# Kernel optimization log

Measured on AMD Instinct MI355X. Metric: run time of the kernel, lower is better.

Reference implementation:

```python
import jax, jax.numpy as jnp
import numpy as np
from jax import lax

B, HI, WI, D = 8, 64, 64, 128
HO, WO = HI // 2, WI // 2
N_IN, N_OUT = HI * WI, HO * WO
NUM_ITERS = 3
EPS = 1e-6


def _build_indices(Ho, Wo):
    # replicates _build_q_and_in_idx: per coarse position, 9 relative offsets
    dys = np.repeat(np.arange(-1, 2), 3)
    dxs = np.tile(np.arange(-1, 2), 3)
    oy = np.arange(Ho)[:, None, None]
    ox = np.arange(Wo)[None, :, None]
    ny = oy + dys
    nx = ox + dxs
    valid = (ny >= 0) & (ny < Ho) & (nx >= 0) & (nx < Wo)  # (Ho,Wo,9)
    coarse = np.where(valid, ny * Wo + nx, 0)
    base = (oy * Wo + ox) * 9
    g9 = np.where(valid, base + np.arange(9), 0).reshape(-1, 9)
    c9 = coarse.reshape(-1, 9)
    q_idx = np.stack([np.tile(g9, (1, 4))] * 4)
    col_idx = np.stack([np.tile(c9, (1, 4))] * 4)
    in_idx = np.stack([np.tile(np.where(valid, coarse * 4 + h, 0).reshape(-1, 9), (1, 4)) for h in range(4)])
    return q_idx.astype(np.int32), in_idx.astype(np.int32), col_idx.astype(np.int32)


Q_IDX, IN_IDX, COL_IDX = _build_indices(HO, WO)
# NATTEN kernel-3 neighborhoods: window center clamped to stay in-bounds.
NY = np.clip(np.arange(HO) - 1, 0, HO - 3)[:, None] + np.arange(3)  # (HO,3)
NX = np.clip(np.arange(WO) - 1, 0, WO - 3)[:, None] + np.arange(3)  # (WO,3)


def _ln(x, g, b, eps=1e-5):
    mu = x.mean(-1, keepdims=True)
    var = ((x - mu) ** 2).mean(-1, keepdims=True)
    return (x - mu) * lax.rsqrt(var + eps) * g + b


def _forward(x, seed_w, wq, wk, wv, w1, b1, w2, b2, ln_in_g, ln_in_b, ln_out_g, ln_out_b, rpb, tau):
    ny, nx = jnp.asarray(NY), jnp.asarray(NX)
    q_idx = jnp.asarray(Q_IDX)

    def unfold(t):  # (B,HI,WI,D) -> (B,4,HO,WO,D); head = ky*2+kx (F.unfold order)
        return t.reshape(B, HO, 2, WO, 2, D).transpose(0, 2, 4, 1, 3, 5).reshape(B, 4, HO, WO, D)

    k = unfold((_ln(x, ln_in_g, ln_in_b) @ wk.T).reshape(B, HI, WI, D))
    v = unfold((x @ wv.T).reshape(B, HI, WI, D))
    k_n = k[:, :, ny][:, :, :, :, nx]  # (B,4,HO,3,WO,3,D)
    v_n = v[:, :, ny][:, :, :, :, nx]

    x_map = x.reshape(B, HI, WI, D).transpose(0, 3, 1, 2)
    seed = lax.conv_general_dilated(x_map, seed_w, (2, 2), ((1, 1), (1, 1)),
                                    dimension_numbers=('NCHW', 'OIHW', 'NCHW'))
    x_out = _ln(seed.reshape(B, D, N_OUT).transpose(0, 2, 1), ln_out_g, ln_out_b)

    scale = jnp.exp(tau)
    attn36 = a_col_h = None
    for _ in range(NUM_ITERS):
        q = (_ln(x_out, ln_out_g, ln_out_b) @ wq.T).reshape(B, HO, WO, D)
        # na2d_qk (q broadcast over the 4 heads) + relative position bias
        logits = jnp.einsum('byxd,bhykxld->bhyxkl', q, k_n).reshape(B, 4, HO, WO, 9) + rpb.reshape(1, 4, 1, 1, 9)
        attn = jax.nn.softmax(logits * scale, axis=-1) + EPS
        flat = attn.reshape(B, 4, N_OUT * 9)
        attn36 = jnp.take_along_axis(
            flat, jnp.broadcast_to(q_idx.reshape(1, 4, -1), (B, 4, N_OUT * 36)), axis=-1
        ).reshape(B, 4, N_OUT, 36)
        a_col_h = attn36 / (attn36.sum(axis=(1, 3), keepdims=True) + EPS)
        attn9 = a_col_h[..., :9].reshape(B, 4, HO, WO, 3, 3)
        # na2d_av then sum over heads
        updates = jnp.einsum('bhyxkl,bhykxld->byxd', attn9, v_n).reshape(B, N_OUT, D)
        x_out = x_out + updates
        h1 = jax.nn.gelu(x_out @ w1.T + b1, approximate=False)
        x_out = x_out + _ln(h1 @ w2.T + b2, ln_out_g, ln_out_b)
    return x_out, attn36, a_col_h


def setup_inputs() -> dict:
    key = jax.random.key(0)
    ks = jax.random.split(key, 8)
    n = lambda k, shape, s: jax.random.normal(k, shape, jnp.float32) * s
    D2 = 2 * D
    return {
        'x': jax.random.normal(ks[0], (B, N_IN, D), jnp.float32),
        'seed_w': n(ks[1], (D, D, 3, 3), (2.0 / (9 * D)) ** 0.5),
        'wq': n(ks[2], (D, D), D ** -0.5),
        'wk': n(ks[3], (D, D), D ** -0.5),
        'wv': n(ks[4], (D, D), D ** -0.5),
        'w1': n(ks[5], (D2, D), D ** -0.5),
        'b1': jnp.zeros((D2,), jnp.float32),
        'w2': n(ks[6], (D, D2), D2 ** -0.5),
        'b2': jnp.zeros((D,), jnp.float32),
        'ln_in_g': jnp.ones((D,), jnp.float32),
        'ln_in_b': jnp.zeros((D,), jnp.float32),
        'ln_out_g': jnp.ones((D,), jnp.float32),
        'ln_out_b': jnp.zeros((D,), jnp.float32),
        'rpb': n(ks[7], (4, 9), 0.02),
        'tau': jnp.float32(np.log(D ** -0.5)),
    }


def reference(x, seed_w, wq, wk, wv, w1, b1, w2, b2, ln_in_g, ln_in_b, ln_out_g, ln_out_b, rpb, tau):
    x_out, attn36, a_col_h = _forward(x, seed_w, wq, wk, wv, w1, b1, w2, b2,
                                      ln_in_g, ln_in_b, ln_out_g, ln_out_b, rpb, tau)
    # A_col: scatter_add over dim 1 -> A_col[b, in_idx[i,j], j] += a_col_h[b,i,j]
    rows = jnp.asarray(IN_IDX).reshape(4 * N_OUT, 36)
    cols = jnp.broadcast_to(jnp.arange(36), rows.shape)
    A_col = jnp.zeros((B, N_IN, N_OUT), x.dtype).at[:, rows, cols].add(a_col_h.reshape(B, 4 * N_OUT, 36))
    # A_row: scatter_add over dim 2 -> A_row[b, i, col_idx[i,j]] += attn36[b,i,j]
    ri = jnp.broadcast_to(jnp.arange(4 * N_OUT)[:, None], (4 * N_OUT, 36))
    A_row = jnp.zeros((B, N_IN, N_OUT), x.dtype).at[:, ri, jnp.asarray(COL_IDX).reshape(4 * N_OUT, 36)].add(
        attn36.reshape(B, 4 * N_OUT, 36))
    return x_out, A_row, A_col
```

## Files before the change

kernel.cpp:

```cpp
#include <hip/hip_runtime.h>
#include <hip/hip_bf16.h>
#include <math.h>

#define BB   8
#define HI_  64
#define WI_  64
#define DD   128
#define HO_  32
#define WO_  32
#define NIN  4096
#define NOUT 1024
#define LN_EPS 1e-5f
#define ATT_EPS 1e-6f

#define ZSHARE 3932160

typedef short bf16x8 __attribute__((ext_vector_type(8)));
typedef float f32x4  __attribute__((ext_vector_type(4)));

__device__ __forceinline__ ushort f2bf(float f) {
    union { float f; unsigned u; } a; a.f = f;
    unsigned u = a.u;
    return (ushort)((u + 0x7FFFu + ((u >> 16) & 1u)) >> 16);
}
__device__ __forceinline__ float bf2f(ushort u) {
    union { unsigned u; float f; } a; a.u = ((unsigned)u) << 16;
    return a.f;
}

__global__ __launch_bounds__(256)
void wconvert_kernel(const float* __restrict__ wq, const float* __restrict__ wk,
                     const float* __restrict__ wv, const float* __restrict__ w1,
                     const float* __restrict__ w2, const float* __restrict__ sw,
                     ushort* __restrict__ dst)
{
    int i = blockIdx.x * 256 + threadIdx.x;
    float v;
    if (i < 16384)        v = wk[i];
    else if (i < 32768)   v = wv[i - 16384];
    else if (i < 49152) { int j = i - 32768; int d = j >> 7, n = j & 127;
                          v = wq[n * DD + d]; }
    else if (i < 81920)   v = w1[i - 49152];
    else if (i < 114688)  v = w2[i - 81920];
    else {
        int j = i - 114688;
        int n = j / 1152;
        int rem = j - n * 1152;
        int tap = rem >> 7, di = rem & 127;
        v = sw[((size_t)(n * DD + di)) * 9 + tap];
    }
    dst[i] = f2bf(v);
}

__global__ __launch_bounds__(256)
void prep_kernel(const float* __restrict__ x, const ushort* __restrict__ wkb,
                 const ushort* __restrict__ wvb, const ushort* __restrict__ wqTb,
                 const ushort* __restrict__ wcb,
                 const float* __restrict__ ligg, const float* __restrict__ libb,
                 const float* __restrict__ logg, const float* __restrict__ lobb,
                 ushort* __restrict__ k2buf, ushort* __restrict__ vbuf,
                 float* __restrict__ xout, float4* __restrict__ zb)
{
    __shared__ __align__(16) char arena[35328];
    const int tid = threadIdx.x;
    const int wid = tid >> 6, lane = tid & 63;
    const int lr = lane & 15, lk = (lane >> 4) << 3;

    {
        float4* zp = zb + (size_t)blockIdx.x * 3840;
        float4 zz = make_float4(0.f, 0.f, 0.f, 0.f);
        #pragma unroll
        for (int i = 0; i < 15; ++i) zp[i * 256 + tid] = zz;
    }

    if (blockIdx.x < 512) {
        ushort (*Araw)[136] = (ushort (*)[136])(arena);
        ushort (*Aln)[136]  = (ushort (*)[136])(arena + 17408);
        const int row0 = blockIdx.x * 64;

        #pragma unroll
        for (int i = 0; i < 8; ++i) {
            int l = tid + i * 256;
            int r = l >> 5, c4 = (l & 31) << 2;
            float4 v = *(const float4*)(x + (size_t)(row0 + r) * DD + c4);
            ushort4 o; o.x = f2bf(v.x); o.y = f2bf(v.y); o.z = f2bf(v.z); o.w = f2bf(v.w);
            *(ushort4*)&Araw[r][c4] = o;
            float s  = v.x + v.y + v.z + v.w;
            float s2 = v.x * v.x + v.y * v.y + v.z * v.z + v.w * v.w;
            #pragma unroll
            for (int o2 = 16; o2 > 0; o2 >>= 1) {
                s  += __shfl_down(s,  o2, 32);
                s2 += __shfl_down(s2, o2, 32);
            }
            s  = __shfl(s,  0, 32);
            s2 = __shfl(s2, 0, 32);
            float mu = s * (1.f / DD);
            float rs = rsqrtf(s2 * (1.f / DD) - mu * mu + LN_EPS);
            ushort4 o2v;
            o2v.x = f2bf((v.x - mu) * rs * ligg[c4 + 0] + libb[c4 + 0]);
            o2v.y = f2bf((v.y - mu) * rs * ligg[c4 + 1] + libb[c4 + 1]);
            o2v.z = f2bf((v.z - mu) * rs * ligg[c4 + 2] + libb[c4 + 2]);
            o2v.w = f2bf((v.w - mu) * rs * ligg[c4 + 3] + libb[c4 + 3]);
            *(ushort4*)&Aln[r][c4] = o2v;
        }
        __syncthreads();

        const int wm = (wid & 1) * 32, wn = (wid >> 1) * 64;
        {
            f32x4 ak[2][4] = {}, av[2][4] = {};
            #pragma unroll
            for (int ks = 0; ks < 4; ++ks) {
                int kk = ks * 32 + lk;
                bf16x8 aL[2], aR[2];
                #pragma unroll
                for (int mi = 0; mi < 2; ++mi) {
                    aL[mi] = *(const bf16x8*)&Aln[wm + mi * 16 + lr][kk];
                    aR[mi] = *(const bf16x8*)&Araw[wm + mi * 16 + lr][kk];
                }
                #pragma unroll
                for (int ni = 0; ni < 4; ++ni) {
                    bf16x8 bK = *(const bf16x8*)(wkb + (size_t)(wn + ni * 16 + lr) * DD + kk);
                    bf16x8 bV = *(const bf16x8*)(wvb + (size_t)(wn + ni * 16 + lr) * DD + kk);
                    #pragma unroll
                    for (int mi = 0; mi < 2; ++mi) {
                        ak[mi][ni] = __builtin_amdgcn_mfma_f32_16x16x32_bf16(aL[mi], bK, ak[mi][ni], 0, 0, 0);
                        av[mi][ni] = __builtin_amdgcn_mfma_f32_16x16x32_bf16(aR[mi], bV, av[mi][ni], 0, 0, 0);
                    }
                }
            }
            #pragma unroll
            for (int mi = 0; mi < 2; ++mi)
                #pragma unroll
                for (int ni = 0; ni < 4; ++ni) {
                    int n = wn + ni * 16 + (lane & 15);
                    #pragma unroll
                    for (int r = 0; r < 4; ++r) {
                        int m = row0 + wm + mi * 16 + ((lane >> 4) << 2) + r;
                        int b = m >> 12, pix = m & 4095;
                        int iy = pix >> 6, ix = pix & 63;
                        int h = ((iy & 1) << 1) | (ix & 1);
                        int cp = ((iy >> 1) << 5) | (ix >> 1);
                        size_t orow = ((size_t)(b * 4 + h) << 10) + cp;
                        vbuf[orow * DD + n] = f2bf(av[mi][ni][r]);
                    }
                }
            __syncthreads();
            #pragma unroll
            for (int mi = 0; mi < 2; ++mi)
                #pragma unroll
                for (int ni = 0; ni < 4; ++ni) {
                    int n = wn + ni * 16 + (lane & 15);
                    #pragma unroll
                    for (int r = 0; r < 4; ++r) {
                        int lm = wm + mi * 16 + ((lane >> 4) << 2) + r;
                        Aln[lm][n] = f2bf(ak[mi][ni][r]);
                    }
                }
        }
        __syncthreads();

        {
            f32x4 a2[2][4] = {};
            #pragma unroll
            for (int ks = 0; ks < 4; ++ks) {
                int kk = ks * 32 + lk;
                bf16x8 aF[2];
                aF[0] = *(const bf16x8*)&Aln[wm + lr][kk];
                aF[1] = *(const bf16x8*)&Aln[wm + 16 + lr][kk];
                #pragma unroll
                for (int ni = 0; ni < 4; ++ni) {
                    bf16x8 bF = *(const bf16x8*)(wqTb + (size_t)(wn + ni * 16 + lr) * DD + kk);
                    a2[0][ni] = __builtin_amdgcn_mfma_f32_16x16x32_bf16(aF[0], bF, a2[0][ni], 0, 0, 0);
                    a2[1][ni] = __builtin_amdgcn_mfma_f32_16x16x32_bf16(aF[1], bF, a2[1][ni], 0, 0, 0);
                }
            }
            #pragma unroll
            for (int mi = 0; mi < 2; ++mi)
                #pragma unroll
                for (int ni = 0; ni < 4; ++ni) {
                    int n = wn + ni * 16 + (lane & 15);
                    #pragma unroll
                    for (int r = 0; r < 4; ++r) {
                        int m = row0 + wm + mi * 16 + ((lane >> 4) << 2) + r;
                        int b = m >> 12, pix = m & 4095;
                        int iy = pix >> 6, ix = pix & 63;
                        int h = ((iy & 1) << 1) | (ix & 1);
                        int cp = ((iy >> 1) << 5) | (ix >> 1);
                        size_t orow = ((size_t)(b * 4 + h) << 10) + cp;
                        k2buf[orow * DD + n] = f2bf(a2[mi][ni][r]);
                    }
                }
        }
    } else {
        ushort (*As)[72]   = (ushort (*)[72])(arena);
        ushort (*Bs)[72]   = (ushort (*)[72])(arena + 2304);
        float  (*es)[132]  = (float  (*)[132])(arena + 20736);
        float  (*rstat)[2] = (float  (*)[2])(arena + 29184);
        const int row0 = (blockIdx.x - 512) * 16;
        const int wn = wid * 32;
        f32x4 acc[2] = {};

        for (int k0 = 0; k0 < 1152; k0 += 64) {
            {
                int r = tid >> 4, c4 = (tid & 15) << 2;
                int m = row0 + r;
                int b = m >> 10, p = m & 1023;
                int y = p >> 5, xx = p & 31;
                int kg = k0 + c4;
                int tap = kg >> 7, di = kg & 127;
                int ky = tap / 3, kx = tap - ky * 3;
                int iy = 2 * y + ky - 1, ix = 2 * xx + kx - 1;
                float4 v;
                if ((unsigned)iy < (unsigned)HI_ && (unsigned)ix < (unsigned)WI_)
                    v = *(const float4*)(x + ((size_t)b * NIN + iy * WI_ + ix) * DD + di);
                else v = make_float4(0.f, 0.f, 0.f, 0.f);
                ushort4 o; o.x = f2bf(v.x); o.y = f2bf(v.y); o.z = f2bf(v.z); o.w = f2bf(v.w);
                *(ushort4*)&As[r][c4] = o;
            }
            #pragma unroll
            for (int i = 0; i < 4; ++i) {
                int l = tid + i * 256;
                int r = l >> 3, c8 = (l & 7) << 3;
                *(uint4*)&Bs[r][c8] = *(const uint4*)(wcb + (size_t)r * 1152 + k0 + c8);
            }
            __syncthreads();
            #pragma unroll
            for (int ks = 0; ks < 2; ++ks) {
                int kk = ks * 32 + lk;
                bf16x8 a0 = *(const bf16x8*)&As[lr][kk];
                #pragma unroll
                for (int ni = 0; ni < 2; ++ni) {
                    bf16x8 bF = *(const bf16x8*)&Bs[wn + ni * 16 + lr][kk];
                    acc[ni] = __builtin_amdgcn_mfma_f32_16x16x32_bf16(a0, bF, acc[ni], 0, 0, 0);
                }
            }
            __syncthreads();
        }
        #pragma unroll
        for (int ni = 0; ni < 2; ++ni) {
            int n = wn + ni * 16 + (lane & 15);
            #pragma unroll
            for (int r = 0; r < 4; ++r)
                es[((lane >> 4) << 2) + r][n] = acc[ni][r];
        }
        __syncthreads();
        if (tid < 64) {
            int r = tid >> 2, q = tid & 3;
            float s = 0.f, s2 = 0.f;
            #pragma unroll
            for (int c = 0; c < 32; ++c) { float v = es[r][q * 32 + c]; s += v; s2 += v * v; }
            s += __shfl_down(s, 1, 64); s2 += __shfl_down(s2, 1, 64);
            s += __shfl_down(s, 2, 64); s2 += __shfl_down(s2, 2, 64);
            if (q == 0) {
                float mu = s * (1.f / DD);
                float var = s2 * (1.f / DD) - mu * mu;
                rstat[r][0] = mu; rstat[r][1] = rsqrtf(var + LN_EPS);
            }
        }
        __syncthreads();
        #pragma unroll
        for (int i = 0; i < 2; ++i) {
            int l = tid + i * 256;
            int r = l >> 5, c4 = (l & 31) << 2;
            float mu = rstat[r][0], rs = rstat[r][1];
            float4 o;
            o.x = (es[r][c4 + 0] - mu) * rs * logg[c4 + 0] + lobb[c4 + 0];
            o.y = (es[r][c4 + 1] - mu) * rs * logg[c4 + 1] + lobb[c4 + 1];
            o.z = (es[r][c4 + 2] - mu) * rs * logg[c4 + 2] + lobb[c4 + 2];
            o.w = (es[r][c4 + 3] - mu) * rs * logg[c4 + 3] + lobb[c4 + 3];
            *(float4*)(xout + (size_t)(row0 + r) * DD + c4) = o;
        }
    }
}

template<int LAST>
__global__ __launch_bounds__(256, 4)
void iter_kernel(float* __restrict__ xout, const ushort* __restrict__ k2buf,
                 const ushort* __restrict__ vbuf,
                 const ushort* __restrict__ w1b, const ushort* __restrict__ w2b,
                 const float* __restrict__ b1, const float* __restrict__ b2,
                 const float* __restrict__ lg_, const float* __restrict__ lb_,
                 const float* __restrict__ rpb, const float* __restrict__ tau,
                 float* __restrict__ gbuf, float* __restrict__ denb,
                 float* __restrict__ out, float4* __restrict__ zb)
{
    const int bid = blockIdx.x;
    const int b = bid >> 6, cy = (bid >> 1) & 31, cx0 = (bid & 1) << 4;
    const int ry0 = min(max(cy - 1, 0), HO_ - 3);
    const int tid = threadIdx.x;
    const int wid = tid >> 6, lane = tid & 63;
    const int lr = lane & 15, lk = (lane >> 4) << 3;

    __shared__ float  xsf[17][132];
    __shared__ ushort qs[17][136];
    __shared__ float  lgp[16][36];
    __shared__ float  lg0[36];
    __shared__ ushort h1s[16][264];
    __shared__ float  es[16][132];
    __shared__ float  fp2[16][4][2];

    {
        float4* zp = zb + (size_t)blockIdx.x * 7680;
        float4 zz = make_float4(0.f, 0.f, 0.f, 0.f);
        #pragma unroll
        for (int i = 0; i < 30; ++i) zp[i * 256 + tid] = zz;
    }

    {
        int c4 = (tid & 31) << 2;
        {
            int r = tid >> 5;
            int g = b * NOUT + cy * 32 + cx0 + r;
            float4 v = *(const float4*)(xout + (size_t)g * DD + c4);
            *(float4*)&xsf[r][c4] = v;
            float s  = v.x + v.y + v.z + v.w;
            float s2 = v.x * v.x + v.y * v.y + v.z * v.z + v.w * v.w;
            #pragma unroll
            for (int o2 = 16; o2 > 0; o2 >>= 1) {
                s  += __shfl_down(s,  o2, 32);
                s2 += __shfl_down(s2, o2, 32);
            }
            s  = __shfl(s,  0, 32);
            s2 = __shfl(s2, 0, 32);
            float mu = s * (1.f / DD);
            float rs = rsqrtf(s2 * (1.f / DD) - mu * mu + LN_EPS);
            ushort4 o;
            o.x = f2bf((v.x - mu) * rs * lg_[c4 + 0] + lb_[c4 + 0]);
            o.y = f2bf((v.y - mu) * rs * lg_[c4 + 1] + lb_[c4 + 1]);
            o.z = f2bf((v.z - mu) * rs * lg_[c4 + 2] + lb_[c4 + 2]);
            o.w = f2bf((v.w - mu) * rs * lg_[c4 + 3] + lb_[c4 + 3]);
            *(ushort4*)&qs[r][c4] = o;
        }
        {
            int r1 = 8 + (tid >> 5);
            int g1 = b * NOUT + cy * 32 + cx0 + r1;
            float4 v = *(const float4*)(xout + (size_t)g1 * DD + c4);
            *(float4*)&xsf[r1][c4] = v;
            float s  = v.x + v.y + v.z + v.w;
            float s2 = v.x * v.x + v.y * v.y + v.z * v.z + v.w * v.w;
            #pragma unroll
            for (int o2 = 16; o2 > 0; o2 >>= 1) {
                s  += __shfl_down(s,  o2, 32);
                s2 += __shfl_down(s2, o2, 32);
            }
            s  = __shfl(s,  0, 32);
            s2 = __shfl(s2, 0, 32);
            float mu = s * (1.f / DD);
            float rs = rsqrtf(s2 * (1.f / DD) - mu * mu + LN_EPS);
            ushort4 o;
            o.x = f2bf((v.x - mu) * rs * lg_[c4 + 0] + lb_[c4 + 0]);
            o.y = f2bf((v.y - mu) * rs * lg_[c4 + 1] + lb_[c4 + 1]);
            o.z = f2bf((v.z - mu) * rs * lg_[c4 + 2] + lb_[c4 + 2]);
            o.w = f2bf((v.w - mu) * rs * lg_[c4 + 3] + lb_[c4 + 3]);
            *(ushort4*)&qs[r1][c4] = o;
        }
        if (tid < 32) {
            int c4c = tid << 2;
            float4 v = *(const float4*)(xout + (size_t)(b * NOUT) * DD + c4c);
            *(float4*)&xsf[16][c4c] = v;
            float s  = v.x + v.y + v.z + v.w;
            float s2 = v.x * v.x + v.y * v.y + v.z * v.z + v.w * v.w;
            #pragma unroll
            for (int o2 = 16; o2 > 0; o2 >>= 1) {
                s  += __shfl_down(s,  o2, 32);
                s2 += __shfl_down(s2, o2, 32);
            }
            s  = __shfl(s,  0, 32);
            s2 = __shfl(s2, 0, 32);
            float mu = s * (1.f / DD);
            float rs = rsqrtf(s2 * (1.f / DD) - mu * mu + LN_EPS);
            ushort4 o;
            o.x = f2bf((v.x - mu) * rs * lg_[c4c + 0] + lb_[c4c + 0]);
            o.y = f2bf((v.y - mu) * rs * lg_[c4c + 1] + lb_[c4c + 1]);
            o.z = f2bf((v.z - mu) * rs * lg_[c4c + 2] + lb_[c4c + 2]);
            o.w = f2bf((v.w - mu) * rs * lg_[c4c + 3] + lb_[c4c + 3]);
            *(ushort4*)&qs[16][c4c] = o;
        }
    }
    __syncthreads();

    for (int task = tid; task < 612; task += 256) {
        const ushort *kp, *qp;
        int cl = 0, h, jj;
        if (task < 576) {
            cl = task / 36; int t2 = task - cl * 36;
            h = t2 / 9; jj = t2 - h * 9;
            int ky = jj / 3, kx = jj - ky * 3;
            int c = cx0 + cl;
            int nx = min(max(c - 1, 0), WO_ - 3) + kx;
            kp = k2buf + (((size_t)(b * 4 + h) << 10) + (ry0 + ky) * 32 + nx) * DD;
            qp = &qs[cl][0];
        } else {
            int t2 = task - 576;
            h = t2 / 9; jj = t2 - h * 9;
            int ky = jj / 3, kx = jj - ky * 3;
            kp = k2buf + (((size_t)(b * 4 + h) << 10) + ky * 32 + kx) * DD;
            qp = &qs[16][0];
        }
        float s = 0.f;
        #pragma unroll 4
        for (int d = 0; d < 128; d += 8) {
            uint4 ku = *(const uint4*)(kp + d);
            uint4 qu = *(const uint4*)(qp + d);
            const ushort* kk2 = (const ushort*)&ku;
            const ushort* qq2 = (const ushort*)&qu;
            #pragma unroll
            for (int t = 0; t < 8; ++t) s += bf2f(kk2[t]) * bf2f(qq2[t]);
        }
        if (task < 576) lgp[cl][h * 9 + jj] = s;
        else            lg0[task - 576] = s;
    }
    __syncthreads();

    if (tid < 64) {
        int cl = tid >> 2, h = tid & 3;
        int c = cx0 + cl;
        float scale = expf(tau[0]);
        float tmpv[9], mx = -1e30f;
        #pragma unroll
        for (int jj = 0; jj < 9; ++jj) {
            float v = (lgp[cl][h * 9 + jj] + rpb[h * 9 + jj]) * scale;
            tmpv[jj] = v; mx = fmaxf(mx, v);
        }
        float ss = 0.f;
        #pragma unroll
        for (int jj = 0; jj < 9; ++jj) { tmpv[jj] = expf(tmpv[jj] - mx); ss += tmpv[jj]; }
        float inv = 1.f / ss;
        float t0[9], mx0 = -1e30f;
        #pragma unroll
        for (int jj = 0; jj < 9; ++jj) {
            float v = (lg0[h * 9 + jj] + rpb[h * 9 + jj]) * scale;
            t0[jj] = v; mx0 = fmaxf(mx0, v);
        }
        float ss0 = 0.f;
        #pragma unroll
        for (int jj = 0; jj < 9; ++jj) ss0 += expf(t0[jj] - mx0);
        float sm0v = expf(t0[0] - mx0) / ss0 + ATT_EPS;
        float s = 0.f, gv[9];
        #pragma unroll
        for (int jj = 0; jj < 9; ++jj) {
            int dy = jj / 3 - 1, dx = jj % 3 - 1;
            bool valid = ((unsigned)(cy + dy) < (unsigned)HO_) && ((unsigned)(c + dx) < (unsigned)WO_);
            float v = valid ? (tmpv[jj] * inv + ATT_EPS) : sm0v;
            gv[jj] = v; s += v;
        }
        float tot = s;
        tot += __shfl_xor(tot, 1, 4);
        tot += __shfl_xor(tot, 2, 4);
        float dd = 4.f * tot + ATT_EPS;
        if (h == 0) denb[b * NOUT + cy * 32 + cx0 + cl] = dd;
        float invd = 1.f / dd;
        float* gp = gbuf + (((size_t)(b * 4 + h) << 10) + cy * 32 + c) * 9;
        #pragma unroll
        for (int jj = 0; jj < 9; ++jj) {
            gp[jj] = gv[jj];
            lgp[cl][h * 9 + jj] = gv[jj] * invd;
        }
    }
    __syncthreads();

    {
        int cl = tid >> 4, d0 = (tid & 15) << 3;
        int c = cx0 + cl;
        int rx0 = min(max(c - 1, 0), WO_ - 3);
        float acc8[8] = {};
        #pragma unroll
        for (int h = 0; h < 4; ++h)
            #pragma unroll
            for (int jj = 0; jj < 9; ++jj) {
                float cf = lgp[cl][h * 9 + jj];
                int ky = jj / 3, kx = jj - ky * 3;
                const ushort* vp = vbuf + (((size_t)(b * 4 + h) << 10) + (ry0 + ky) * 32 + rx0 + kx) * DD + d0;
                uint4 v0 = *(const uint4*)(vp);
                const ushort* vs0 = (const ushort*)&v0;
                #pragma unroll
                for (int t = 0; t < 8; ++t) acc8[t] += cf * bf2f(vs0[t]);
            }
        float nv[8];
        #pragma unroll
        for (int t = 0; t < 8; ++t) nv[t] = xsf[cl][d0 + t] + acc8[t];
        #pragma unroll
        for (int t = 0; t < 8; t += 4)
            *(float4*)&xsf[cl][d0 + t] = make_float4(nv[t], nv[t+1], nv[t+2], nv[t+3]);
        ushort4 q0, q1;
        q0.x = f2bf(nv[0]); q0.y = f2bf(nv[1]); q0.z = f2bf(nv[2]); q0.w = f2bf(nv[3]);
        q1.x = f2bf(nv[4]); q1.y = f2bf(nv[5]); q1.z = f2bf(nv[6]); q1.w = f2bf(nv[7]);
        *(ushort4*)&qs[cl][d0]     = q0;
        *(ushort4*)&qs[cl][d0 + 4] = q1;
    }
    __syncthreads();

    {
        const int wn = wid * 64;
        f32x4 acc[4] = {};
        #pragma unroll
        for (int ks = 0; ks < 4; ++ks) {
            int kk = ks * 32 + lk;
            bf16x8 a0 = *(const bf16x8*)&qs[lr][kk];
            #pragma unroll
            for (int ni = 0; ni < 4; ++ni) {
                bf16x8 bF = *(const bf16x8*)(w1b + (size_t)(wn + ni * 16 + lr) * DD + kk);
                acc[ni] = __builtin_amdgcn_mfma_f32_16x16x32_bf16(a0, bF, acc[ni], 0, 0, 0);
            }
        }
        #pragma unroll
        for (int ni = 0; ni < 4; ++ni) {
            int n = wn + ni * 16 + (lane & 15);
            float bv = b1[n];
            #pragma unroll
            for (int r = 0; r < 4; ++r) {
                int m = ((lane >> 4) << 2) + r;
                float v = acc[ni][r] + bv;
                v = 0.5f * v * (1.f + erff(v * 0.70710678118654752f));
                h1s[m][n] = f2bf(v);
            }
        }
    }
    __syncthreads();

    {
        const int wn = wid * 32;
        f32x4 acc[2] = {};
        #pragma unroll
        for (int ks = 0; ks < 8; ++ks) {
            int kk = ks * 32 + lk;
            bf16x8 a0 = *(const bf16x8*)&h1s[lr][kk];
            #pragma unroll
            for (int ni = 0; ni < 2; ++ni) {
                bf16x8 bF = *(const bf16x8*)(w2b + (size_t)(wn + ni * 16 + lr) * 256 + kk);
                acc[ni] = __builtin_amdgcn_mfma_f32_16x16x32_bf16(a0, bF, acc[ni], 0, 0, 0);
            }
        }
        float bv0 = b2[wn + (lane & 15)];
        float bv1 = b2[wn + 16 + (lane & 15)];
        #pragma unroll
        for (int r = 0; r < 4; ++r) {
            int m = ((lane >> 4) << 2) + r;
            float v0 = acc[0][r] + bv0;
            float v1 = acc[1][r] + bv1;
            es[m][wn + (lane & 15)] = v0;
            es[m][wn + 16 + (lane & 15)] = v1;
            float s = v0 + v1, s2 = v0 * v0 + v1 * v1;
            #pragma unroll
            for (int o = 1; o < 16; o <<= 1) {
                s  += __shfl_down(s,  o, 16);
                s2 += __shfl_down(s2, o, 16);
            }
            if ((lane & 15) == 0) { fp2[m][wid][0] = s; fp2[m][wid][1] = s2; }
        }
    }
    __syncthreads();
    for (int l = tid; l < 512; l += 256) {
        int r = l >> 5, c4 = (l & 31) << 2;
        float s  = fp2[r][0][0] + fp2[r][1][0] + fp2[r][2][0] + fp2[r][3][0];
        float s2 = fp2[r][0][1] + fp2[r][1][1] + fp2[r][2][1] + fp2[r][3][1];
        float mu = s * (1.f / DD);
        float rs = rsqrtf(s2 * (1.f / DD) - mu * mu + LN_EPS);
        size_t off = ((size_t)(b * NOUT + cy * 32 + cx0 + r)) * DD + c4;
        float4 o;
        o.x = xsf[r][c4 + 0] + (es[r][c4 + 0] - mu) * rs * lg_[c4 + 0] + lb_[c4 + 0];
        o.y = xsf[r][c4 + 1] + (es[r][c4 + 1] - mu) * rs * lg_[c4 + 1] + lb_[c4 + 1];
        o.z = xsf[r][c4 + 2] + (es[r][c4 + 2] - mu) * rs * lg_[c4 + 2] + lb_[c4 + 2];
        o.w = xsf[r][c4 + 3] + (es[r][c4 + 3] - mu) * rs * lg_[c4 + 3] + lb_[c4 + 3];
        if (LAST) *(float4*)(out + off) = o;
        else      *(float4*)(xout + off) = o;
    }
}

__global__ __launch_bounds__(256)
void sparse_finish_kernel(const float* __restrict__ gbuf, const float* __restrict__ denb,
                          float* __restrict__ Arow, float* __restrict__ Acol)
{
    const int tid = threadIdx.x;
    if (blockIdx.x < 128) {
        int row = blockIdx.x * 256 + tid;
        int b = row >> 12, i = row & 4095;
        int h = i >> 10, p = i & 1023;
        int cy = p >> 5, cx = p & 31;
        const float* gp = gbuf + (((size_t)(b * 4 + h) << 10) + p) * 9;
        float* rowp = Arow + (size_t)row * NOUT;
        float acc0 = 0.f; bool has0 = false;
        #pragma unroll
        for (int jj = 0; jj < 9; ++jj) {
            int dy = jj / 3 - 1, dx = jj % 3 - 1;
            bool valid = ((unsigned)(cy + dy) < (unsigned)HO_) && ((unsigned)(cx + dx) < (unsigned)WO_);
            float g4 = 4.f * gp[jj];
            int col = (cy + dy) * WO_ + (cx + dx);
            if (valid && col != 0) rowp[col] = g4;
            else { acc0 += g4; has0 = true; }
        }
        if (has0) rowp[0] = acc0;
    } else if (blockIdx.x < 240) {
        int br = (blockIdx.x - 128) * 256 + tid;
        int b = br >> 12, r = br & 4095;
        if (r != 0) {
            int h = r & 3, coarse = r >> 2;
            int cy = coarse >> 5, cx = coarse & 31;
            float val[9];
            #pragma unroll
            for (int jj = 0; jj < 9; ++jj) {
                int dy = jj / 3 - 1, dx = jj % 3 - 1;
                int py = cy - dy, px = cx - dx;
                float v = 0.f;
                if ((unsigned)py < (unsigned)HO_ && (unsigned)px < (unsigned)WO_) {
                    int p = py * WO_ + px;
                    v = gbuf[(((size_t)(b * 4 + h) << 10) + p) * 9 + jj] / denb[b * NOUT + p];
                }
                val[jj] = v;
            }
            float* rowp = Acol + (size_t)br * NOUT;
            #pragma unroll
            for (int q = 0; q < 9; ++q) {
                float4 o = make_float4(val[(4 * q) % 9], val[(4 * q + 1) % 9],
                                       val[(4 * q + 2) % 9], val[(4 * q + 3) % 9]);
                *(float4*)(rowp + 4 * q) = o;
            }
        }
    } else if (blockIdx.x < 247) {
        const int b = blockIdx.x - 240;
        __shared__ float vals[9];
        __shared__ float wred[9][4];
        if (tid < 9) {
            int dy = tid / 3 - 1, dx = tid % 3 - 1;
            int py = -dy, px = -dx;
            float v = 0.f;
            if ((unsigned)py < (unsigned)HO_ && (unsigned)px < (unsigned)WO_) {
                int p = py * WO_ + px;
                v = gbuf[(((size_t)(b * 4 + 0) << 10) + p) * 9 + tid] / denb[b * NOUT + p];
            }
            vals[tid] = v;
        }
        float part[9] = {};
        for (int p = tid; p < NOUT; p += 256) {
            float invd = 1.f / denb[b * NOUT + p];
            int py = p >> 5, px = p & 31;
            #pragma unroll
            for (int jj = 0; jj < 9; ++jj) {
                int dy = jj / 3 - 1, dx = jj % 3 - 1;
                bool valid = ((unsigned)(py + dy) < (unsigned)HO_) && ((unsigned)(px + dx) < (unsigned)WO_);
                if (!valid) part[jj] += invd;
            }
        }
        #pragma unroll
        for (int jj = 0; jj < 9; ++jj) {
            float s = part[jj];
            #pragma unroll
            for (int o = 32; o > 0; o >>= 1) s += __shfl_down(s, o, 64);
            if ((tid & 63) == 0) wred[jj][tid >> 6] = s;
        }
        __syncthreads();
        if (tid < 9) {
            float s = wred[tid][0] + wred[tid][1] + wred[tid][2] + wred[tid][3];
            float H = 0.f;
            for (int h2 = 0; h2 < 4; ++h2)
                H += gbuf[(((size_t)(b * 4 + h2)) << 10) * 9];
            vals[tid] += H * s;
        }
        __syncthreads();
        if (tid < 36) Acol[(size_t)(b * 4096) * NOUT + tid] = vals[tid % 9];
    } else {
        const int br = 28672 + (blockIdx.x - 247);
        const int b = br >> 12, r = br & 4095;
        const int h = r & 3, coarse = r >> 2;
        const int cy = coarse >> 5, cx = coarse & 31;
        __shared__ float vals[9];
        __shared__ float wred[9][4];
        if (tid < 9) {
            int dy = tid / 3 - 1, dx = tid % 3 - 1;
            int py = cy - dy, px = cx - dx;
            float v = 0.f;
            if ((unsigned)py < (unsigned)HO_ && (unsigned)px < (unsigned)WO_) {
                int p = py * WO_ + px;
                v = gbuf[(((size_t)(b * 4 + h) << 10) + p) * 9 + tid] / denb[b * NOUT + p];
            }
            vals[tid] = v;
        }
        if (r == 0) {
            float part[9] = {};
            for (int p = tid; p < NOUT; p += 256) {
                float invd = 1.f / denb[b * NOUT + p];
                int py = p >> 5, px = p & 31;
                #pragma unroll
                for (int jj = 0; jj < 9; ++jj) {
                    int dy = jj / 3 - 1, dx = jj % 3 - 1;
                    bool valid = ((unsigned)(py + dy) < (unsigned)HO_) && ((unsigned)(px + dx) < (unsigned)WO_);
                    if (!valid) part[jj] += invd;
                }
            }
            #pragma unroll
            for (int jj = 0; jj < 9; ++jj) {
                float s = part[jj];
                #pragma unroll
                for (int o = 32; o > 0; o >>= 1) s += __shfl_down(s, o, 64);
                if ((tid & 63) == 0) wred[jj][tid >> 6] = s;
            }
            __syncthreads();
            if (tid < 9) {
                float s = wred[tid][0] + wred[tid][1] + wred[tid][2] + wred[tid][3];
                float H = 0.f;
                for (int h2 = 0; h2 < 4; ++h2)
                    H += gbuf[(((size_t)(b * 4 + h2)) << 10) * 9];
                vals[tid] += H * s;
            }
        }
        __syncthreads();
        float* rowp = Acol + (size_t)br * NOUT;
        int c4 = tid << 2;
        float o[4];
        #pragma unroll
        for (int e = 0; e < 4; ++e) {
            int c = c4 + e;
            o[e] = (c < 36) ? vals[c % 9] : 0.f;
        }
        *(float4*)(rowp + c4) = make_float4(o[0], o[1], o[2], o[3]);
    }
}

extern "C" void kernel_launch(void* const* d_in, const int* in_sizes, int n_in,
                              void* d_out, int out_size, void* d_ws, size_t ws_size,
                              hipStream_t stream)
{
    const float* x        = (const float*)d_in[0];
    const float* seed_w   = (const float*)d_in[1];
    const float* wq       = (const float*)d_in[2];
    const float* wk       = (const float*)d_in[3];
    const float* wv       = (const float*)d_in[4];
    const float* w1       = (const float*)d_in[5];
    const float* b1       = (const float*)d_in[6];
    const float* w2       = (const float*)d_in[7];
    const float* b2       = (const float*)d_in[8];
    const float* ln_in_g  = (const float*)d_in[9];
    const float* ln_in_b  = (const float*)d_in[10];
    const float* ln_out_g = (const float*)d_in[11];
    const float* ln_out_b = (const float*)d_in[12];
    const float* rpb      = (const float*)d_in[13];
    const float* tau      = (const float*)d_in[14];

    float* out  = (float*)d_out;
    float* Arow = out + (size_t)BB * NOUT * DD;
    float* Acol = Arow + (size_t)BB * NIN * NOUT;
    float4* zb  = (float4*)Arow;

    float* ws    = (float*)d_ws;
    float* xout  = ws;
    float* gbuf  = xout + (size_t)BB * NOUT * DD;
    float* denb  = gbuf + (size_t)BB * 4 * NOUT * 9;
    ushort* wb   = (ushort*)(denb + BB * NOUT);
    ushort* wkb  = wb;
    ushort* wvb  = wb + 16384;
    ushort* wqTb = wb + 32768;
    ushort* w1b  = wb + 49152;
    ushort* w2b  = wb + 81920;
    ushort* wcb  = wb + 114688;

    ushort* k2buf = (ushort*)(Acol + (size_t)28672 * NOUT);
    ushort* vbuf  = k2buf + (size_t)4194304;

    wconvert_kernel<<<1024, 256, 0, stream>>>(wq, wk, wv, w1, w2, seed_w, wb);
    prep_kernel<<<1024, 256, 0, stream>>>(x, wkb, wvb, wqTb, wcb, ln_in_g, ln_in_b,
                                          ln_out_g, ln_out_b, k2buf, vbuf, xout,
                                          zb + (size_t)0 * ZSHARE);

    iter_kernel<0><<<BB * HO_ * 2, 256, 0, stream>>>(
        xout, k2buf, vbuf, w1b, w2b, b1, b2, ln_out_g, ln_out_b,
        rpb, tau, gbuf, denb, out, zb + (size_t)1 * ZSHARE);
    iter_kernel<0><<<BB * HO_ * 2, 256, 0, stream>>>(
        xout, k2buf, vbuf, w1b, w2b, b1, b2, ln_out_g, ln_out_b,
        rpb, tau, gbuf, denb, out, zb + (size_t)2 * ZSHARE);
    iter_kernel<1><<<BB * HO_ * 2, 256, 0, stream>>>(
        xout, k2buf, vbuf, w1b, w2b, b1, b2, ln_out_g, ln_out_b,
        rpb, tau, gbuf, denb, out, zb + (size_t)3 * ZSHARE);

    sparse_finish_kernel<<<4343, 256, 0, stream>>>(gbuf, denb, Arow, Acol);
}
```

Baseline: 157.2 us.

## Compute neighborhood q·k logits with MFMA tiles instead of scalar dot products

Replaces the per-thread scalar bf16 dot-product loop for the 576 neighborhood logits with MFMA 16x16x32 tiles. Each wave handles (head, key row) pairs, multiplying the query rows against a full 32-wide key row, then scatters only the in-window 3 columns into lgp. This computes many unused products and pads the query tile to 32 rows, enlarging qs shared memory. It aims to cut VALU work and repeated key loads. The 36 seed logits still use the scalar path.

```diff
diff --git a/kernel.cpp b/kernel.cpp
--- a/kernel.cpp
+++ b/kernel.cpp
@@ -292,7 +292,7 @@
     const int lr = lane & 15, lk = (lane >> 4) << 3;
 
     __shared__ float  xsf[17][132];
-    __shared__ ushort qs[17][136];
+    __shared__ ushort qs[32][136];
     __shared__ float  lgp[16][36];
     __shared__ float  lg0[36];
     __shared__ ushort h1s[16][264];
@@ -379,36 +379,60 @@
     }
     __syncthreads();
 
-    for (int task = tid; task < 612; task += 256) {
-        const ushort *kp, *qp;
-        int cl = 0, h, jj;
-        if (task < 576) {
-            cl = task / 36; int t2 = task - cl * 36;
-            h = t2 / 9; jj = t2 - h * 9;
+    {
+        #pragma unroll
+        for (int pi = 0; pi < 3; ++pi) {
+            int pair = wid * 3 + pi;
+            int h = pair / 3, ky = pair - h * 3;
+            const ushort* krowbase = k2buf +
+                ((((size_t)(b * 4 + h)) << 10) + (ry0 + ky) * 32) * DD;
+            f32x4 acc[2][2] = {};
+            #pragma unroll
+            for (int ks = 0; ks < 4; ++ks) {
+                int kk = ks * 32 + lk;
+                bf16x8 aF0 = *(const bf16x8*)&qs[lr][kk];
+                bf16x8 aF1 = *(const bf16x8*)&qs[16 + lr][kk];
+                #pragma unroll
+                for (int ni = 0; ni < 2; ++ni) {
+                    bf16x8 bF = *(const bf16x8*)(krowbase + (size_t)(ni * 16 + lr) * DD + kk);
+                    acc[0][ni] = __builtin_amdgcn_mfma_f32_16x16x32_bf16(aF0, bF, acc[0][ni], 0, 0, 0);
+                    acc[1][ni] = __builtin_amdgcn_mfma_f32_16x16x32_bf16(aF1, bF, acc[1][ni], 0, 0, 0);
+                }
+            }
+            #pragma unroll
+            for (int mi = 0; mi < 2; ++mi)
+                #pragma unroll
+                for (int ni = 0; ni < 2; ++ni) {
+                    int col = ni * 16 + (lane & 15);
+                    #pragma unroll
+                    for (int r = 0; r < 4; ++r) {
+                        int qrow = mi * 16 + ((lane >> 4) << 2) + r;
+                        if (qrow < 16) {
+                            int base = min(max(cx0 + qrow - 1, 0), WO_ - 3);
+                            int kx = col - base;
+                            if ((unsigned)kx < 3u)
+                                lgp[qrow][h * 9 + ky * 3 + kx] = acc[mi][ni][r];
+                        }
+                    }
+                }
+        }
+        if (tid < 36) {
+            int h = tid / 9, jj = tid - h * 9;
             int ky = jj / 3, kx = jj - ky * 3;
-            int c = cx0 + cl;
-            int nx = min(max(c - 1, 0), WO_ - 3) + kx;
-            kp = k2buf + (((size_t)(b * 4 + h) << 10) + (ry0 + ky) * 32 + nx) * DD;
-            qp = &qs[cl][0];
-        } else {
-            int t2 = task - 576;
-            h = t2 / 9; jj = t2 - h * 9;
-            int ky = jj / 3, kx = jj - ky * 3;
-            kp = k2buf + (((size_t)(b * 4 + h) << 10) + ky * 32 + kx) * DD;
-            qp = &qs[16][0];
-        }
-        float s = 0.f;
-        #pragma unroll 4
-        for (int d = 0; d < 128; d += 8) {
-            uint4 ku = *(const uint4*)(kp + d);
-            uint4 qu = *(const uint4*)(qp + d);
-            const ushort* kk2 = (const ushort*)&ku;
-            const ushort* qq2 = (const ushort*)&qu;
-            #pragma unroll
-            for (int t = 0; t < 8; ++t) s += bf2f(kk2[t]) * bf2f(qq2[t]);
-        }
-        if (task < 576) lgp[cl][h * 9 + jj] = s;
-        else            lg0[task - 576] = s;
+            const ushort* kp = k2buf + ((((size_t)(b * 4 + h)) << 10) + ky * 32 + kx) * DD;
+            const ushort* qp = &qs[16][0];
+            float s = 0.f;
+            #pragma unroll 4
+            for (int d = 0; d < 128; d += 8) {
+                uint4 ku = *(const uint4*)(kp + d);
+                uint4 qu = *(const uint4*)(qp + d);
+                const ushort* kk2 = (const ushort*)&ku;
+                const ushort* qq2 = (const ushort*)&qu;
+                #pragma unroll
+                for (int t = 0; t < 8; ++t) s += bf2f(kk2[t]) * bf2f(qq2[t]);
+            }
+            lg0[tid] = s;
+        }
     }
     __syncthreads();
 
```

After: 160.8 us. +2.3%, slower.
